# Kernel optimization log

Measured on AMD Instinct MI355X. Metric: run time of the kernel, lower is better.

The kernel has to match this reference:

```python
import jax, jax.numpy as jnp
import numpy as np

NUM_PER_SCALE = (64, 64, 64)   # static num_intervals_per_scale
DIST_BINS = 21
NUM_CLASSES = 5
D = 128   # node_embedding_dim
N = 512   # number of nodes (time frames)
KSIZE = 5


def _gru_last(x_seq, lens, Wih, Whh, bih, bhh):
    """Masked GRU over padded seqs; final hidden at each sequence's true length.
    x_seq: [I, T, F], lens: [I]. PyTorch GRU cell math."""
    I, T, _ = x_seq.shape
    H = Whh.shape[1]
    mask_t = (jnp.arange(T)[None, :] < lens[:, None]).T  # [T, I]

    def step(h, inp):
        x_t, m = inp
        gi = x_t @ Wih.T + bih            # [I, 3H]
        gh = h @ Whh.T + bhh
        ir, iz, in_ = jnp.split(gi, 3, axis=-1)
        hr, hz, hn = jnp.split(gh, 3, axis=-1)
        r = jax.nn.sigmoid(ir + hr)
        z = jax.nn.sigmoid(iz + hz)
        n = jnp.tanh(in_ + r * hn)
        h_new = (1.0 - z) * n + z * h
        return jnp.where(m[:, None], h_new, h), None

    h0 = jnp.zeros((I, H), x_seq.dtype)
    h_fin, _ = jax.lax.scan(step, h0, (jnp.swapaxes(x_seq, 0, 1), mask_t))
    return h_fin


def _bigru_last(x_pad, lens, Wih, Whh, bih, bhh):
    """Bidirectional GRU final hiddens, matching packed-sequence semantics."""
    hf = _gru_last(x_pad, lens, Wih[0], Whh[0], bih[0], bhh[0])
    T = x_pad.shape[1]
    t = jnp.arange(T)[None, :]
    rev = jnp.where(t < lens[:, None], lens[:, None] - 1 - t, t)  # reverse within valid length
    x_rev = jnp.take_along_axis(x_pad, rev[:, :, None], axis=1)
    hb = _gru_last(x_rev, lens, Wih[1], Whh[1], bih[1], bhh[1])
    return hf, hb


def reference(node_embeddings, time_positions, node_pred, audio_len,
              cur_anchor_intervals, smooth_kernel,
              feat_Wih, feat_Whh, feat_bih, feat_bhh,
              abn_Wih, abn_Whh, abn_bih, abn_bhh,
              start_w, end_w,
              uni_W1, uni_b1, uni_W2, uni_b2, uni_W3, uni_b3):
    n, d = node_embeddings.shape
    al = audio_len
    # temporal encoding
    freqs = jnp.linspace(0.0, 10.0, d)
    x = node_embeddings + 0.05 * jnp.sin(time_positions * freqs)  # [N, D]
    # grouped gaussian smoothing over time per class channel (symmetric kernel)
    pad = KSIZE // 2
    xp = jnp.pad(node_pred, ((pad, pad), (0, 0)))
    win = jnp.stack([xp[k:k + n] for k in range(KSIZE)])          # [K, N, C]
    smoothed = jax.nn.softmax(jnp.einsum('k,knc->nc', smooth_kernel, win), axis=-1)
    abnormal = smoothed[:, 0]                                     # normal_class_idx = 0
    tpos = time_positions[:, 0] * al                              # [N]

    bounds_list, conf_list, cls_list = [], [], []
    off = 0
    for s in range(3):
        ni = NUM_PER_SCALE[s]
        anc = cur_anchor_intervals[off:off + ni]
        off += ni
        starts, ends = anc[:, 0], anc[:, 1]
        mask = (tpos[None, :] >= starts[:, None]) & (tpos[None, :] <= ends[:, None])  # [ni, N]
        lens = mask.sum(axis=1)
        # stable gather: in-interval nodes first, original node order preserved
        key = jnp.where(mask, 0, n) + jnp.arange(n)[None, :]
        order = jnp.argsort(key, axis=1)
        x_pad = x[order]                       # [ni, N, D]
        abn_pad = abnormal[order][:, :, None]  # [ni, N, 1]
        hf, hb = _bigru_last(x_pad, lens, feat_Wih[s], feat_Whh[s], feat_bih[s], feat_bhh[s])
        af, ab = _bigru_last(abn_pad, lens, abn_Wih[s], abn_Whh[s], abn_bih[s], abn_bhh[s])
        local_feat = jnp.concatenate([hf, hb], axis=1)             # [ni, 2D]
        local_abn = (af[:, 0] + ab[:, 0]) * 0.5
        centers = (starts + ends) * 0.5
        widths = ends - starts
        sf = jnp.concatenate([local_feat, local_abn[:, None],
                              (centers / al)[:, None], (widths / al)[:, None]], axis=1)
        h = jax.nn.relu(sf @ uni_W1[s] + uni_b1[s])
        h = jax.nn.relu(h @ uni_W2[s] + uni_b2[s])   # dropout inactive (eval)
        out = h @ uni_W3[s] + uni_b3[s]
        sl = out[:, :DIST_BINS]
        el = out[:, DIST_BINS:2 * DIST_BINS]
        conf = out[:, 2 * DIST_BINS]
        cls = out[:, 2 * DIST_BINS + 1:]
        so = jax.nn.softmax(sl, axis=1) @ start_w[s]
        eo = jax.nn.softmax(el, axis=1) @ end_w[s]
        st = jnp.clip(starts + so, 0.0, al)
        en = jnp.clip(ends + eo, 0.0, al)
        bounds_list.append(jnp.stack([st, en], axis=1))
        conf_list.append(conf)
        cls_list.append(cls)
    return (jnp.concatenate(bounds_list, 0),
            jnp.concatenate(conf_list, 0),
            jnp.concatenate(cls_list, 0))


def setup_inputs():
    key = jax.random.key(0)
    ks = jax.random.split(key, 16)
    node_embeddings = jax.random.normal(ks[0], (N, D), dtype=jnp.float32)
    time_positions = jax.random.uniform(ks[1], (N, 1), dtype=jnp.float32)
    node_pred = jax.random.normal(ks[2], (N, NUM_CLASSES), dtype=jnp.float32)
    audio_len = jnp.ones((), jnp.float32)
    total = sum(NUM_PER_SCALE)
    st = jax.random.uniform(ks[3], (total,), minval=0.0, maxval=0.75)
    wd = jax.random.uniform(ks[4], (total,), minval=0.05, maxval=0.2)
    cur_anchor_intervals = jnp.stack([st, jnp.minimum(st + wd, 1.0)], axis=1)
    smooth_kernel = jnp.array([0.06136, 0.24477, 0.38774, 0.24477, 0.06136], jnp.float32)
    feat_Wih = 0.05 * jax.random.normal(ks[5], (3, 2, 3 * D, D))
    feat_Whh = 0.05 * jax.random.normal(ks[6], (3, 2, 3 * D, D))
    feat_bih = 0.05 * jax.random.normal(ks[7], (3, 2, 3 * D))
    feat_bhh = 0.05 * jax.random.normal(ks[8], (3, 2, 3 * D))
    abn_Wih = 0.5 * jax.random.normal(ks[9], (3, 2, 3, 1))
    abn_Whh = 0.5 * jax.random.normal(ks[10], (3, 2, 3, 1))
    abn_bih = 0.5 * jax.random.normal(ks[11], (3, 2, 3))
    abn_bhh = 0.5 * jax.random.normal(ks[12], (3, 2, 3))
    lin = jnp.linspace(-20.0, 20.0, DIST_BINS)
    start_w = jnp.tile(lin[None, :], (3, 1))
    end_w = jnp.tile(lin[None, :], (3, 1))
    fin = 2 * D + 3
    fout = 2 * DIST_BINS + 1 + (NUM_CLASSES - 1)
    uni_W1 = jax.random.normal(ks[13], (3, fin, 256)) / float(np.sqrt(fin))
    uni_b1 = jnp.zeros((3, 256), jnp.float32)
    uni_W2 = jax.random.normal(ks[14], (3, 256, 256)) / 16.0
    uni_b2 = jnp.zeros((3, 256), jnp.float32)
    uni_W3 = jax.random.normal(ks[15], (3, 256, fout)) / 16.0
    uni_b3 = jnp.zeros((3, fout), jnp.float32)
    return dict(node_embeddings=node_embeddings, time_positions=time_positions,
                node_pred=node_pred, audio_len=audio_len,
                cur_anchor_intervals=cur_anchor_intervals, smooth_kernel=smooth_kernel,
                feat_Wih=feat_Wih, feat_Whh=feat_Whh, feat_bih=feat_bih, feat_bhh=feat_bhh,
                abn_Wih=abn_Wih, abn_Whh=abn_Whh, abn_bih=abn_bih, abn_bhh=abn_bhh,
                start_w=start_w, end_w=end_w,
                uni_W1=uni_W1, uni_b1=uni_b1, uni_W2=uni_W2, uni_b2=uni_b2,
                uni_W3=uni_W3, uni_b3=uni_b3)
```

## Files before the change

kernel.cpp:

```cpp
#include <hip/hip_runtime.h>
#include <math.h>

#define N_NODES 512
#define DIM 128
#define NANCH 192
#define G3 384
#define FOUT 47
#define DBINS 21

__device__ __forceinline__ float fast_sigmoid(float x) {
    return __builtin_amdgcn_rcpf(1.f + __expf(-x));
}
__device__ __forceinline__ float fast_tanh(float x) {
    return 1.f - 2.f * __builtin_amdgcn_rcpf(1.f + __expf(2.f * x));
}

__global__ __launch_bounds__(128) void prep_kernel(
    const float* __restrict__ emb, const float* __restrict__ tpin,
    const float* __restrict__ npred, const float* __restrict__ alp,
    const float* __restrict__ skern,
    float* __restrict__ x, float* __restrict__ abnormal, float* __restrict__ tpos)
{
    int n = blockIdx.x;
    int d = threadIdx.x;
    float tv = tpin[n];
    float freq = 10.f * (float)d / 127.f;
    x[n * DIM + d] = emb[n * DIM + d] + 0.05f * __sinf(tv * freq);
    if (d == 0) {
        tpos[n] = tv * alp[0];
        float sc[5];
        #pragma unroll
        for (int c = 0; c < 5; ++c) {
            float acc = 0.f;
            #pragma unroll
            for (int k = 0; k < 5; ++k) {
                int r = n + k - 2;
                if (r >= 0 && r < N_NODES) acc += skern[k] * npred[r * 5 + c];
            }
            sc[c] = acc;
        }
        float m = sc[0];
        #pragma unroll
        for (int c = 1; c < 5; ++c) m = fmaxf(m, sc[c]);
        float sum = 0.f;
        #pragma unroll
        for (int c = 0; c < 5; ++c) sum += __expf(sc[c] - m);
        abnormal[n] = __expf(sc[0] - m) / sum;
    }
}

__global__ __launch_bounds__(384) void xw_gemm_kernel(
    const float* __restrict__ x, const float* __restrict__ Wih,
    const float* __restrict__ bih, float* __restrict__ xW)
{
    int blk = blockIdx.x;
    int sd = blk >> 5;
    int ng = blk & 31;
    int tid = threadIdx.x;
    __shared__ __align__(16) float xs[16][DIM];
    for (int idx = tid; idx < 16 * DIM; idx += 384) {
        int m = idx >> 7, k = idx & 127;
        xs[m][k] = x[(ng * 16 + m) * DIM + k];
    }
    __syncthreads();
    float acc[16];
    float b = bih[sd * G3 + tid];
    #pragma unroll
    for (int m = 0; m < 16; ++m) acc[m] = b;
    const float* wrow = Wih + ((size_t)sd * G3 + tid) * DIM;
    for (int k = 0; k < DIM; k += 4) {
        float4 w4 = *(const float4*)(wrow + k);
        #pragma unroll
        for (int m = 0; m < 16; ++m) {
            float4 xv = *(const float4*)&xs[m][k];
            acc[m] = fmaf(w4.x, xv.x, acc[m]);
            acc[m] = fmaf(w4.y, xv.y, acc[m]);
            acc[m] = fmaf(w4.z, xv.z, acc[m]);
            acc[m] = fmaf(w4.w, xv.w, acc[m]);
        }
    }
    #pragma unroll
    for (int m = 0; m < 16; ++m)
        xW[((size_t)sd * N_NODES + ng * 16 + m) * G3 + tid] = acc[m];
}

__global__ __launch_bounds__(64) void membership_abn_kernel(
    const float* __restrict__ tpos, const float* __restrict__ anchors,
    const float* __restrict__ abnormal,
    const float* __restrict__ aWih, const float* __restrict__ aWhh,
    const float* __restrict__ abih, const float* __restrict__ abhh,
    int* __restrict__ members, int* __restrict__ lens, float* __restrict__ abn_res)
{
    int a = blockIdx.x;
    int lane = threadIdx.x;
    float s0 = anchors[a * 2 + 0];
    float e0 = anchors[a * 2 + 1];
    __shared__ int memloc[N_NODES];
    int count = 0;
    for (int c = 0; c < N_NODES / 64; ++c) {
        int node = c * 64 + lane;
        float tp = tpos[node];
        bool in = (tp >= s0) && (tp <= e0);
        unsigned long long m = __ballot(in);
        if (in) {
            int pos = count + __popcll(m & ((1ull << lane) - 1ull));
            members[a * N_NODES + pos] = node;
            memloc[pos] = node;
        }
        count += __popcll(m);
    }
    if (lane == 0) lens[a] = count;
    __syncthreads();
    int sc = a >> 6;
    float h = 0.f;
    if (lane < 2) {
        int sd = sc * 2 + lane;
        float wi0 = aWih[sd * 3 + 0], wi1 = aWih[sd * 3 + 1], wi2 = aWih[sd * 3 + 2];
        float wh0 = aWhh[sd * 3 + 0], wh1 = aWhh[sd * 3 + 1], wh2 = aWhh[sd * 3 + 2];
        float bi0 = abih[sd * 3 + 0], bi1 = abih[sd * 3 + 1], bi2 = abih[sd * 3 + 2];
        float bh0 = abhh[sd * 3 + 0], bh1 = abhh[sd * 3 + 1], bh2 = abhh[sd * 3 + 2];
        for (int t = 0; t < count; ++t) {
            int idx = lane ? (count - 1 - t) : t;
            float xv = abnormal[memloc[idx]];
            float r = fast_sigmoid(fmaf(wi0, xv, bi0) + fmaf(wh0, h, bh0));
            float z = fast_sigmoid(fmaf(wi1, xv, bi1) + fmaf(wh1, h, bh1));
            float nv = fast_tanh(fmaf(wi2, xv, bi2) + r * fmaf(wh2, h, bh2));
            h = (1.f - z) * nv + z * h;
        }
    }
    float hb = __shfl(h, 1);
    if (lane == 0) abn_res[a] = 0.5f * (h + hb);
}

__global__ __launch_bounds__(512, 2) void gru_feat_kernel(
    const float* __restrict__ xW, const float* __restrict__ Whh,
    const float* __restrict__ bhh, const int* __restrict__ members,
    const int* __restrict__ lens, float* __restrict__ feat_out)
{
    int b = blockIdx.x;
    int a = b >> 1;
    int dir = b & 1;
    int s3 = a >> 6;
    int sd = s3 * 2 + dir;
    int t0 = threadIdx.x;
    int j  = t0 >> 2;
    int s  = t0 & 3;

    float wr[32], wz[32], wn[32];
    {
        const float* base = Whh + ((size_t)sd * G3) * DIM;
        const float* pr = base + (size_t)(j        ) * DIM + s * 32;
        const float* pz = base + (size_t)(j + DIM  ) * DIM + s * 32;
        const float* pn = base + (size_t)(j + 2*DIM) * DIM + s * 32;
        #pragma unroll
        for (int q = 0; q < 8; ++q) {
            float4 v = *(const float4*)(pr + 4 * q);
            wr[4*q+0]=v.x; wr[4*q+1]=v.y; wr[4*q+2]=v.z; wr[4*q+3]=v.w;
        }
        #pragma unroll
        for (int q = 0; q < 8; ++q) {
            float4 v = *(const float4*)(pz + 4 * q);
            wz[4*q+0]=v.x; wz[4*q+1]=v.y; wz[4*q+2]=v.z; wz[4*q+3]=v.w;
        }
        #pragma unroll
        for (int q = 0; q < 8; ++q) {
            float4 v = *(const float4*)(pn + 4 * q);
            wn[4*q+0]=v.x; wn[4*q+1]=v.y; wn[4*q+2]=v.z; wn[4*q+3]=v.w;
        }
    }
    float bhr = bhh[sd * G3 + j];
    float bhz = bhh[sd * G3 + DIM + j];
    float bhn = bhh[sd * G3 + 2 * DIM + j];

    const float* xWp = xW + (size_t)sd * N_NODES * G3;
    const int* mem = members + a * N_NODES;
    int len = lens[a];

    __shared__ __align__(16) float hbuf[2][4][36];
    for (int i = t0; i < 2 * 4 * 36; i += 512) ((float*)hbuf)[i] = 0.f;
    __syncthreads();

    int node = (len > 0) ? mem[dir ? (len - 1) : 0] : 0;
    float gr = xWp[(size_t)node * G3 + j];
    float gz = xWp[(size_t)node * G3 + DIM + j];
    float gn = xWp[(size_t)node * G3 + 2 * DIM + j];

    int cur = 0;
    for (int t = 0; t < len; ++t) {
        float gr_n = 0.f, gz_n = 0.f, gn_n = 0.f;
        if (t + 1 < len) {
            int nn = mem[dir ? (len - 2 - t) : (t + 1)];
            gr_n = xWp[(size_t)nn * G3 + j];
            gz_n = xWp[(size_t)nn * G3 + DIM + j];
            gn_n = xWp[(size_t)nn * G3 + 2 * DIM + j];
        }
        float ar = 0.f, az = 0.f, an_ = 0.f;
        const float4* hp = (const float4*)(&hbuf[cur][s][0]);
        #pragma unroll
        for (int q = 0; q < 8; ++q) {
            float4 hv = hp[q];
            ar = fmaf(wr[4*q+0], hv.x, ar); ar = fmaf(wr[4*q+1], hv.y, ar);
            ar = fmaf(wr[4*q+2], hv.z, ar); ar = fmaf(wr[4*q+3], hv.w, ar);
            az = fmaf(wz[4*q+0], hv.x, az); az = fmaf(wz[4*q+1], hv.y, az);
            az = fmaf(wz[4*q+2], hv.z, az); az = fmaf(wz[4*q+3], hv.w, az);
            an_ = fmaf(wn[4*q+0], hv.x, an_); an_ = fmaf(wn[4*q+1], hv.y, an_);
            an_ = fmaf(wn[4*q+2], hv.z, an_); an_ = fmaf(wn[4*q+3], hv.w, an_);
        }
        ar  += __shfl_xor(ar, 1);  ar  += __shfl_xor(ar, 2);
        az  += __shfl_xor(az, 1);  az  += __shfl_xor(az, 2);
        an_ += __shfl_xor(an_, 1); an_ += __shfl_xor(an_, 2);

        float r  = fast_sigmoid(gr + ar + bhr);
        float z  = fast_sigmoid(gz + az + bhz);
        float nv = fast_tanh(gn + r * (an_ + bhn));
        float hj = hbuf[cur][j >> 5][j & 31];
        float hnew = (1.f - z) * nv + z * hj;
        if (s == 0) hbuf[cur ^ 1][j >> 5][j & 31] = hnew;
        __syncthreads();
        cur ^= 1;
        gr = gr_n; gz = gz_n; gn = gn_n;
    }
    if (s == 0) feat_out[a * 256 + dir * DIM + j] = hbuf[cur][j >> 5][j & 31];
}

__global__ __launch_bounds__(256) void head_kernel(
    const float* __restrict__ feat, const float* __restrict__ abn_res,
    const float* __restrict__ anchors, const float* __restrict__ alp,
    const float* __restrict__ W1, const float* __restrict__ b1,
    const float* __restrict__ W2, const float* __restrict__ b2,
    const float* __restrict__ W3, const float* __restrict__ b3,
    const float* __restrict__ sw, const float* __restrict__ ew,
    float* __restrict__ out)
{
    int a = blockIdx.x;
    int tid = threadIdx.x;
    int s = a >> 6;
    __shared__ float sf[259];
    __shared__ float h1[256];
    __shared__ float h2[256];
    __shared__ float o[FOUT];
    float al = alp[0];
    float st = anchors[a * 2 + 0];
    float en = anchors[a * 2 + 1];
    sf[tid] = feat[a * 256 + tid];
    if (tid == 0) {
        sf[256] = abn_res[a];
        sf[257] = (st + en) * 0.5f / al;
        sf[258] = (en - st) / al;
    }
    __syncthreads();

    const float* w1 = W1 + (size_t)s * 259 * 256;
    float acc = b1[s * 256 + tid];
    for (int jj = 0; jj < 259; ++jj) acc = fmaf(sf[jj], w1[jj * 256 + tid], acc);
    h1[tid] = fmaxf(acc, 0.f);
    __syncthreads();

    const float* w2 = W2 + (size_t)s * 256 * 256;
    acc = b2[s * 256 + tid];
    for (int jj = 0; jj < 256; ++jj) acc = fmaf(h1[jj], w2[jj * 256 + tid], acc);
    h2[tid] = fmaxf(acc, 0.f);
    __syncthreads();

    if (tid < FOUT) {
        const float* w3 = W3 + (size_t)s * 256 * FOUT;
        acc = b3[s * FOUT + tid];
        for (int jj = 0; jj < 256; ++jj) acc = fmaf(h2[jj], w3[jj * FOUT + tid], acc);
        o[tid] = acc;
    }
    __syncthreads();

    if (tid < 2) {
        const float* lw = (tid == 0) ? (sw + s * DBINS) : (ew + s * DBINS);
        const float* sl = o + tid * DBINS;
        float m = sl[0];
        for (int jj = 1; jj < DBINS; ++jj) m = fmaxf(m, sl[jj]);
        float sum = 0.f, dot = 0.f;
        for (int jj = 0; jj < DBINS; ++jj) {
            float e = __expf(sl[jj] - m);
            sum += e;
            dot = fmaf(e, lw[jj], dot);
        }
        float off = dot / sum;
        float base = (tid == 0) ? st : en;
        out[a * 2 + tid] = fminf(fmaxf(base + off, 0.f), al);
    }
    if (tid == 42) out[2 * NANCH + a] = o[42];
    if (tid >= 43 && tid < FOUT) out[3 * NANCH + a * 4 + (tid - 43)] = o[tid];
}

extern "C" void kernel_launch(void* const* d_in, const int* in_sizes, int n_in,
                              void* d_out, int out_size, void* d_ws, size_t ws_size,
                              hipStream_t stream) {
    const float* emb   = (const float*)d_in[0];
    const float* tpin  = (const float*)d_in[1];
    const float* npred = (const float*)d_in[2];
    const float* alp   = (const float*)d_in[3];
    const float* anch  = (const float*)d_in[4];
    const float* skern = (const float*)d_in[5];
    const float* fWih  = (const float*)d_in[6];
    const float* fWhh  = (const float*)d_in[7];
    const float* fbih  = (const float*)d_in[8];
    const float* fbhh  = (const float*)d_in[9];
    const float* aWih  = (const float*)d_in[10];
    const float* aWhh  = (const float*)d_in[11];
    const float* abih  = (const float*)d_in[12];
    const float* abhh  = (const float*)d_in[13];
    const float* sw    = (const float*)d_in[14];
    const float* ew    = (const float*)d_in[15];
    const float* W1    = (const float*)d_in[16];
    const float* b1    = (const float*)d_in[17];
    const float* W2    = (const float*)d_in[18];
    const float* b2    = (const float*)d_in[19];
    const float* W3    = (const float*)d_in[20];
    const float* b3    = (const float*)d_in[21];

    float* ws = (float*)d_ws;
    float* x        = ws;
    float* xW       = ws + 65536;
    float* abnormal = ws + 1245184;
    float* tpos     = ws + 1245696;
    float* abn_res  = ws + 1246208;
    float* feat     = ws + 1246464;
    int*   members  = (int*)(ws + 1295616);
    int*   lens     = (int*)(ws + 1393920);
    float* outp     = (float*)d_out;

    prep_kernel<<<N_NODES, DIM, 0, stream>>>(emb, tpin, npred, alp, skern, x, abnormal, tpos);
    xw_gemm_kernel<<<6 * 32, 384, 0, stream>>>(x, fWih, fbih, xW);
    membership_abn_kernel<<<NANCH, 64, 0, stream>>>(tpos, anch, abnormal, aWih, aWhh, abih, abhh,
                                                    members, lens, abn_res);
    gru_feat_kernel<<<2 * NANCH, 512, 0, stream>>>(xW, fWhh, fbhh, members, lens, feat);
    head_kernel<<<NANCH, 256, 0, stream>>>(feat, abn_res, anch, alp,
                                           W1, b1, W2, b2, W3, b3, sw, ew, outp);
}
```

Measured before the change: 271.1 us.

## Fuse prep kernel into GEMM and membership kernels; keep GRU hidden in register

Removes the separate prep kernel. The GEMM now computes the temporal encoding inline while staging x into shared memory, and each membership block recomputes the smoothed softmax abnormal scores and time positions itself into LDS. This saves one launch and the global round trips for x, tpos and abnormal, but repeats the small smoothing work in each of the 192 blocks. The GRU feature kernel also keeps h_j in a register instead of re-reading it from LDS, and swaps the min-blocks launch bound for a waves_per_eu attribute.

```diff
diff --git a/kernel.cpp b/kernel.cpp
--- a/kernel.cpp
+++ b/kernel.cpp
@@ -15,43 +15,10 @@
     return 1.f - 2.f * __builtin_amdgcn_rcpf(1.f + __expf(2.f * x));
 }
 
-__global__ __launch_bounds__(128) void prep_kernel(
+__global__ __launch_bounds__(384) void xw_gemm_kernel(
     const float* __restrict__ emb, const float* __restrict__ tpin,
-    const float* __restrict__ npred, const float* __restrict__ alp,
-    const float* __restrict__ skern,
-    float* __restrict__ x, float* __restrict__ abnormal, float* __restrict__ tpos)
-{
-    int n = blockIdx.x;
-    int d = threadIdx.x;
-    float tv = tpin[n];
-    float freq = 10.f * (float)d / 127.f;
-    x[n * DIM + d] = emb[n * DIM + d] + 0.05f * __sinf(tv * freq);
-    if (d == 0) {
-        tpos[n] = tv * alp[0];
-        float sc[5];
-        #pragma unroll
-        for (int c = 0; c < 5; ++c) {
-            float acc = 0.f;
-            #pragma unroll
-            for (int k = 0; k < 5; ++k) {
-                int r = n + k - 2;
-                if (r >= 0 && r < N_NODES) acc += skern[k] * npred[r * 5 + c];
-            }
-            sc[c] = acc;
-        }
-        float m = sc[0];
-        #pragma unroll
-        for (int c = 1; c < 5; ++c) m = fmaxf(m, sc[c]);
-        float sum = 0.f;
-        #pragma unroll
-        for (int c = 0; c < 5; ++c) sum += __expf(sc[c] - m);
-        abnormal[n] = __expf(sc[0] - m) / sum;
-    }
-}
-
-__global__ __launch_bounds__(384) void xw_gemm_kernel(
-    const float* __restrict__ x, const float* __restrict__ Wih,
-    const float* __restrict__ bih, float* __restrict__ xW)
+    const float* __restrict__ Wih, const float* __restrict__ bih,
+    float* __restrict__ xW)
 {
     int blk = blockIdx.x;
     int sd = blk >> 5;
@@ -60,7 +27,10 @@
     __shared__ __align__(16) float xs[16][DIM];
     for (int idx = tid; idx < 16 * DIM; idx += 384) {
         int m = idx >> 7, k = idx & 127;
-        xs[m][k] = x[(ng * 16 + m) * DIM + k];
+        int node = ng * 16 + m;
+        float tv = tpin[node];
+        float freq = 10.f * (float)k / 127.f;
+        xs[m][k] = emb[node * DIM + k] + 0.05f * __sinf(tv * freq);
     }
     __syncthreads();
     float acc[16];
@@ -85,21 +55,48 @@
 }
 
 __global__ __launch_bounds__(64) void membership_abn_kernel(
-    const float* __restrict__ tpos, const float* __restrict__ anchors,
-    const float* __restrict__ abnormal,
+    const float* __restrict__ tpin, const float* __restrict__ alp,
+    const float* __restrict__ anchors,
+    const float* __restrict__ npred, const float* __restrict__ skern,
     const float* __restrict__ aWih, const float* __restrict__ aWhh,
     const float* __restrict__ abih, const float* __restrict__ abhh,
     int* __restrict__ members, int* __restrict__ lens, float* __restrict__ abn_res)
 {
     int a = blockIdx.x;
     int lane = threadIdx.x;
+    float al = alp[0];
     float s0 = anchors[a * 2 + 0];
     float e0 = anchors[a * 2 + 1];
     __shared__ int memloc[N_NODES];
+    __shared__ float abn_lds[N_NODES];
+    float k_[5];
+    #pragma unroll
+    for (int k = 0; k < 5; ++k) k_[k] = skern[k];
+    for (int c = 0; c < N_NODES / 64; ++c) {
+        int node = c * 64 + lane;
+        float sc[5];
+        #pragma unroll
+        for (int ch = 0; ch < 5; ++ch) {
+            float acc = 0.f;
+            #pragma unroll
+            for (int k = 0; k < 5; ++k) {
+                int r = node + k - 2;
+                if (r >= 0 && r < N_NODES) acc += k_[k] * npred[r * 5 + ch];
+            }
+            sc[ch] = acc;
+        }
+        float m = sc[0];
+        #pragma unroll
+        for (int ch = 1; ch < 5; ++ch) m = fmaxf(m, sc[ch]);
+        float sum = 0.f;
+        #pragma unroll
+        for (int ch = 0; ch < 5; ++ch) sum += __expf(sc[ch] - m);
+        abn_lds[node] = __expf(sc[0] - m) / sum;
+    }
     int count = 0;
     for (int c = 0; c < N_NODES / 64; ++c) {
         int node = c * 64 + lane;
-        float tp = tpos[node];
+        float tp = tpin[node] * al;
         bool in = (tp >= s0) && (tp <= e0);
         unsigned long long m = __ballot(in);
         if (in) {
@@ -111,17 +108,17 @@
     }
     if (lane == 0) lens[a] = count;
     __syncthreads();
-    int sc = a >> 6;
+    int sc3 = a >> 6;
     float h = 0.f;
     if (lane < 2) {
-        int sd = sc * 2 + lane;
+        int sd = sc3 * 2 + lane;
         float wi0 = aWih[sd * 3 + 0], wi1 = aWih[sd * 3 + 1], wi2 = aWih[sd * 3 + 2];
         float wh0 = aWhh[sd * 3 + 0], wh1 = aWhh[sd * 3 + 1], wh2 = aWhh[sd * 3 + 2];
         float bi0 = abih[sd * 3 + 0], bi1 = abih[sd * 3 + 1], bi2 = abih[sd * 3 + 2];
         float bh0 = abhh[sd * 3 + 0], bh1 = abhh[sd * 3 + 1], bh2 = abhh[sd * 3 + 2];
         for (int t = 0; t < count; ++t) {
             int idx = lane ? (count - 1 - t) : t;
-            float xv = abnormal[memloc[idx]];
+            float xv = abn_lds[memloc[idx]];
             float r = fast_sigmoid(fmaf(wi0, xv, bi0) + fmaf(wh0, h, bh0));
             float z = fast_sigmoid(fmaf(wi1, xv, bi1) + fmaf(wh1, h, bh1));
             float nv = fast_tanh(fmaf(wi2, xv, bi2) + r * fmaf(wh2, h, bh2));
@@ -132,7 +129,8 @@
     if (lane == 0) abn_res[a] = 0.5f * (h + hb);
 }
 
-__global__ __launch_bounds__(512, 2) void gru_feat_kernel(
+__global__ __attribute__((amdgpu_waves_per_eu(2, 2))) __launch_bounds__(512)
+void gru_feat_kernel(
     const float* __restrict__ xW, const float* __restrict__ Whh,
     const float* __restrict__ bhh, const int* __restrict__ members,
     const int* __restrict__ lens, float* __restrict__ feat_out)
@@ -180,11 +178,12 @@
     for (int i = t0; i < 2 * 4 * 36; i += 512) ((float*)hbuf)[i] = 0.f;
     __syncthreads();
 
-    int node = (len > 0) ? mem[dir ? (len - 1) : 0] : 0;
-    float gr = xWp[(size_t)node * G3 + j];
-    float gz = xWp[(size_t)node * G3 + DIM + j];
-    float gn = xWp[(size_t)node * G3 + 2 * DIM + j];
-
+    int node0 = (len > 0) ? mem[dir ? (len - 1) : 0] : 0;
+    float gr = xWp[(size_t)node0 * G3 + j];
+    float gz = xWp[(size_t)node0 * G3 + DIM + j];
+    float gn = xWp[(size_t)node0 * G3 + 2 * DIM + j];
+
+    float hj = 0.f;
     int cur = 0;
     for (int t = 0; t < len; ++t) {
         float gr_n = 0.f, gz_n = 0.f, gn_n = 0.f;
@@ -213,14 +212,13 @@
         float r  = fast_sigmoid(gr + ar + bhr);
         float z  = fast_sigmoid(gz + az + bhz);
         float nv = fast_tanh(gn + r * (an_ + bhn));
-        float hj = hbuf[cur][j >> 5][j & 31];
-        float hnew = (1.f - z) * nv + z * hj;
-        if (s == 0) hbuf[cur ^ 1][j >> 5][j & 31] = hnew;
+        hj = (1.f - z) * nv + z * hj;
+        if (s == 0) hbuf[cur ^ 1][j >> 5][j & 31] = hj;
         __syncthreads();
         cur ^= 1;
         gr = gr_n; gz = gz_n; gn = gn_n;
     }
-    if (s == 0) feat_out[a * 256 + dir * DIM + j] = hbuf[cur][j >> 5][j & 31];
+    if (s == 0) feat_out[a * 256 + dir * DIM + j] = hj;
 }
 
 __global__ __launch_bounds__(256) void head_kernel(
@@ -316,19 +314,16 @@
     const float* b3    = (const float*)d_in[21];
 
     float* ws = (float*)d_ws;
-    float* x        = ws;
-    float* xW       = ws + 65536;
-    float* abnormal = ws + 1245184;
-    float* tpos     = ws + 1245696;
-    float* abn_res  = ws + 1246208;
-    float* feat     = ws + 1246464;
-    int*   members  = (int*)(ws + 1295616);
-    int*   lens     = (int*)(ws + 1393920);
+    float* xW       = ws;
+    float* abn_res  = ws + 1179648;
+    float* feat     = ws + 1179904;
+    int*   members  = (int*)(ws + 1229056);
+    int*   lens     = (int*)(ws + 1327360);
     float* outp     = (float*)d_out;
 
-    prep_kernel<<<N_NODES, DIM, 0, stream>>>(emb, tpin, npred, alp, skern, x, abnormal, tpos);
-    xw_gemm_kernel<<<6 * 32, 384, 0, stream>>>(x, fWih, fbih, xW);
-    membership_abn_kernel<<<NANCH, 64, 0, stream>>>(tpos, anch, abnormal, aWih, aWhh, abih, abhh,
+    xw_gemm_kernel<<<6 * 32, 384, 0, stream>>>(emb, tpin, fWih, fbih, xW);
+    membership_abn_kernel<<<NANCH, 64, 0, stream>>>(tpin, alp, anch, npred, skern,
+                                                    aWih, aWhh, abih, abhh,
                                                     members, lens, abn_res);
     gru_feat_kernel<<<2 * NANCH, 512, 0, stream>>>(xW, fWhh, fbhh, members, lens, feat);
     head_kernel<<<NANCH, 256, 0, stream>>>(feat, abn_res, anch, alp,
```

Result: slower. 297.1 us (+9.6%).
